# Kernel tuning notes

Hardware: AMD Instinct MI355X
Metric: run time of the kernel (lower is better)

## Reference

```python
import jax, jax.numpy as jnp
import numpy as np

VSN = 1e-12  # VERY_SMALL_NUMBER
B, N, IN_DIM = 48, 512, 400
ENC, HID, OUT, NREL = 256, 128, 128, 53
NUM_PERS, KNN, EPS, SKIP = 4, 10, 0.3, 0.8


def setup_inputs() -> dict:
    key = jax.random.key(0)
    ks = jax.random.split(key, 12)
    context = jax.random.normal(ks[0], (B, N, IN_DIM), dtype=jnp.float32)
    context_lens = jax.random.randint(ks[1], (B,), N // 2, N + 1)
    s1 = jax.random.randint(ks[2], (B,), 0, N - 16)
    e1 = s1 + jax.random.randint(ks[3], (B,), 1, 8)
    s2 = jax.random.randint(ks[4], (B,), 0, N - 16)
    e2 = s2 + jax.random.randint(ks[5], (B,), 1, 8)
    mentions = jnp.stack([s1, e1, s2, e2], axis=-1)  # [B,4]
    sc = lambda d: 1.0 / np.sqrt(d)
    w_enc = jax.random.normal(ks[6], (IN_DIM, ENC), dtype=jnp.float32) * sc(IN_DIM)
    b_enc = jnp.zeros((ENC,), jnp.float32)
    gl_weight = jax.random.normal(ks[7], (NUM_PERS, IN_DIM), dtype=jnp.float32)
    gcn_w1 = jax.random.normal(ks[8], (ENC, HID), dtype=jnp.float32) * sc(ENC)
    gcn_b1 = jnp.zeros((HID,), jnp.float32)
    gcn_w2 = jax.random.normal(ks[9], (HID, OUT), dtype=jnp.float32) * sc(HID)
    gcn_b2 = jnp.zeros((OUT,), jnp.float32)
    lin_w = jax.random.normal(ks[10], (OUT, NREL), dtype=jnp.float32) * sc(OUT)
    lin_b = jnp.zeros((NREL,), jnp.float32)
    return dict(context=context, context_lens=context_lens, mentions=mentions,
                w_enc=w_enc, b_enc=b_enc, gl_weight=gl_weight,
                gcn_w1=gcn_w1, gcn_b1=gcn_b1, gcn_w2=gcn_w2, gcn_b2=gcn_b2,
                lin_w=lin_w, lin_b=lin_b)


def _knn_init_adj(feats, mask):
    # binarized kNN graph on raw features + symmetric normalization
    mask2d = mask[:, :, None] * mask[:, None, :]
    att = jnp.einsum('bnd,bmd->bnm', feats, feats) * mask2d
    _, idx = jax.lax.top_k(att, KNN)                      # [B,N,K]
    adj = jnp.zeros((B, N, N), feats.dtype).at[
        jnp.arange(B)[:, None, None], jnp.arange(N)[None, :, None], idx].set(1.0)
    adj = adj * mask2d
    rowsum = jnp.clip(adj.sum(-1), VSN, None)
    rinv = (rowsum ** -0.5) * mask                        # [B,N]
    return rinv[:, :, None] * adj * rinv[:, None, :]


def _weighted_cosine(feats, gl_weight, mask):
    # multi-perspective weighted cosine similarity, epsilon-sparsified (>=0 adj)
    ctx = feats[None] * gl_weight[:, None, None, :]       # [P,B,N,D]
    ctx = ctx / jnp.clip(jnp.linalg.norm(ctx, axis=-1, keepdims=True), VSN, None)
    att = jnp.einsum('pbnd,pbmd->pbnm', ctx, ctx).mean(0)  # [B,N,N]
    mask2d = mask[:, :, None] * mask[:, None, :]
    att = att * mask2d                                    # markoff_value = 0
    return att * (att > EPS).astype(att.dtype)


def _merge(enc_seq, start, end):
    w_ids = jnp.arange(N)[None, :]                        # [1,N]
    ind = ((w_ids >= start[:, None]) & (w_ids <= end[:, None])).astype(enc_seq.dtype)
    return jnp.einsum('bn,bnd->bd', ind, enc_seq) / ind.sum(-1, keepdims=True)


def reference(context, context_lens, mentions, w_enc, b_enc, gl_weight,
              gcn_w1, gcn_b1, gcn_w2, gcn_b2, lin_w, lin_b):
    mask = (jnp.arange(N)[None, :] < context_lens[:, None]).astype(jnp.float32)
    # init kNN adjacency on detached raw features
    init_adj = _knn_init_adj(jax.lax.stop_gradient(context), mask)
    # context encoder (linear projection stand-in for the LSTM ctx_encoder)
    enc = context @ w_enc + b_enc                          # [B,N,ENC]
    # learned graph: row-normalize then skip-connect with init_adj
    raw_adj = _weighted_cosine(context, gl_weight, mask)
    adj = raw_adj / jnp.clip(raw_adj.sum(-1, keepdims=True), VSN, None)
    adj = SKIP * init_adj + (1.0 - SKIP) * adj
    # 2-hop GCN encoder
    h = jax.nn.relu(jnp.einsum('bnm,bmd->bnd', adj, enc) @ gcn_w1 + gcn_b1)
    node_vec = jnp.einsum('bnm,bmd->bnd', adj, h) @ gcn_w2 + gcn_b2  # [B,N,OUT]
    # graph maxpool over nodes + mention merging (broadcast-mask averaging)
    pooled = node_vec.max(axis=1)                          # [B,OUT]
    arg1 = _merge(node_vec, mentions[:, 0], mentions[:, 1])
    arg2 = _merge(node_vec, mentions[:, 2], mentions[:, 3])
    return (pooled + arg1 + arg2) @ lin_w + lin_b          # [B,NREL]
```

## Files before the change

kernel.cpp:

```cpp
#include <hip/hip_runtime.h>
#include <math.h>

constexpr int cB = 48, cN = 512, cIN = 400;
constexpr int cENC = 256, cHID = 128, cOUT = 128, cNREL = 53;
constexpr int cKNN = 10;
constexpr float cVSN = 1e-12f;
constexpr float cEPS = 0.3f;

constexpr int KP = 416;
constexpr size_t ARRSZ = (size_t)cB * cN * KP;
constexpr int NBN = cB * cN;
constexpr size_t NADJ = (size_t)cB * cN * cN;
constexpr size_t NE1 = (size_t)NBN * 128;

typedef _Float16 f16;
typedef _Float16 f16x8 __attribute__((ext_vector_type(8)));
typedef float f32x4 __attribute__((ext_vector_type(4)));

__device__ inline void gload16(const void* g, void* l) {
    __builtin_amdgcn_global_load_lds(
        (const __attribute__((address_space(1))) unsigned int*)g,
        (__attribute__((address_space(3))) unsigned int*)l, 16, 0, 0);
}

#define MFMA16(a, b, c) __builtin_amdgcn_mfma_f32_16x16x32_f16((a), (b), (c), 0, 0, 0)

__global__ void k_wprep(const float* __restrict__ w_enc, const float* __restrict__ w1,
                        const float* __restrict__ b_enc, const float* __restrict__ w2,
                        f16* __restrict__ wc1H, float* __restrict__ bc1p,
                        f16* __restrict__ w2tH)
{
    int d = blockIdx.x;
    int t = threadIdx.x;
    __shared__ float wred[2][128];
    int o = t & 127, half = t >> 7;
    if (d < cIN) {
        float acc = 0.f;
        const float* we = w_enc + (size_t)d * cENC + half * 128;
        const float* w1p = w1 + (size_t)half * 128 * cHID + o;
        #pragma unroll 8
        for (int e = 0; e < 128; ++e) acc += we[e] * w1p[(size_t)e * cHID];
        wred[half][o] = acc;
        __syncthreads();
        if (half == 0) wc1H[(size_t)o * KP + d] = (f16)(wred[0][o] + wred[1][o]);
    } else if (d < KP) {
        if (t < 128) wc1H[(size_t)o * KP + d] = (f16)0.f;
    } else {
        float acc = 0.f;
        const float* w1p = w1 + (size_t)half * 128 * cHID + o;
        #pragma unroll 8
        for (int e = 0; e < 128; ++e) acc += b_enc[half * 128 + e] * w1p[(size_t)e * cHID];
        wred[half][o] = acc;
        __syncthreads();
        if (half == 0) bc1p[o] = wred[0][o] + wred[1][o];
    }
    if (d < cHID && t < 128) w2tH[(size_t)t * cHID + d] = (f16)w2[(size_t)d * cOUT + t];
}

__global__ __launch_bounds__(256) void k_split(const float* __restrict__ X,
                                               f16* __restrict__ XH, f16* __restrict__ XL)
{
    int t = threadIdx.x;
    int row = blockIdx.x * 4 + (t >> 6);
    int k8 = t & 63;
    if (k8 >= 52) return;
    size_t obase = (size_t)row * KP + k8 * 8;
    if (k8 < 50) {
        const float* x = X + (size_t)row * cIN + k8 * 8;
        float4 xa = *(const float4*)x;
        float4 xb = *(const float4*)(x + 4);
        float xv[8] = {xa.x, xa.y, xa.z, xa.w, xb.x, xb.y, xb.z, xb.w};
        f16x8 vh, vl;
        #pragma unroll
        for (int e = 0; e < 8; ++e) {
            f16 hh = (f16)xv[e];
            vh[e] = hh;
            vl[e] = (f16)(xv[e] - (float)hh);
        }
        *(f16x8*)(XH + obase) = vh;
        *(f16x8*)(XL + obase) = vl;
    } else {
        f16x8 z = (f16x8)(f16)0.f;
        *(f16x8*)(XH + obase) = z;
        *(f16x8*)(XL + obase) = z;
    }
}

__global__ __launch_bounds__(256) void k_norms(const float* __restrict__ X,
                                               const int* __restrict__ lens,
                                               const float* __restrict__ glw,
                                               float* __restrict__ maskA,
                                               float* __restrict__ invnM)
{
    int row = blockIdx.x;
    int t = threadIdx.x;
    int w = t >> 6, lane = t & 63;
    __shared__ float sw[4];
    int b = row >> 9, n = row & (cN - 1);
    float s = 0.f;
    if (lane < 50) {
        int k = lane * 8;
        const float* x = X + (size_t)row * cIN + k;
        const float* g = glw + (size_t)w * cIN + k;
        float4 xa = *(const float4*)x, xb = *(const float4*)(x + 4);
        float4 ga = *(const float4*)g, gb = *(const float4*)(g + 4);
        float xv[8] = {xa.x, xa.y, xa.z, xa.w, xb.x, xb.y, xb.z, xb.w};
        float gv[8] = {ga.x, ga.y, ga.z, ga.w, gb.x, gb.y, gb.z, gb.w};
        #pragma unroll
        for (int e = 0; e < 8; ++e) {
            float tt = xv[e] * gv[e];
            s += tt * tt;
        }
    }
    #pragma unroll
    for (int off = 32; off; off >>= 1) s += __shfl_xor(s, off, 64);
    if (lane == 0) sw[w] = s;
    __syncthreads();
    if (t == 0) {
        float m = (n < lens[b]) ? 1.0f : 0.0f;
        float4 iv;
        iv.x = m / fmaxf(sqrtf(sw[0]), cVSN);
        iv.y = m / fmaxf(sqrtf(sw[1]), cVSN);
        iv.z = m / fmaxf(sqrtf(sw[2]), cVSN);
        iv.w = m / fmaxf(sqrtf(sw[3]), cVSN);
        *(float4*)&invnM[(size_t)row * 4] = iv;
        maskA[row] = m;
    }
}

__global__ __launch_bounds__(256, 3) void k_sim_mfma(
    const f16* __restrict__ XH, const f16* __restrict__ XL,
    const float* __restrict__ glw, const int* __restrict__ lens,
    const float* __restrict__ maskA, const float* __restrict__ invnM,
    float* __restrict__ G0, f16* __restrict__ RAh)
{
    int L = blockIdx.x + (blockIdx.y << 3) + (blockIdx.z << 6);
    int xcd = L & 7, j0 = L >> 3;
    int work = xcd * 384 + j0;
    const int b = work >> 6;
    int rem = work & 63;
    const int n0 = (rem >> 3) * 64, m0 = (rem & 7) * 64;

    const int t = threadIdx.x;
    const int w = t >> 6, lane = t & 63;
    const int wr = w >> 1, wc = w & 1;
    const int lr = lane & 15, lc = lane >> 4;

    const size_t rowBaseB = (size_t)b * cN;
    const int len = lens[b];

    if (n0 >= len || m0 >= len) {
        #pragma unroll
        for (int i = 0; i < 2; ++i)
            #pragma unroll
            for (int jj = 0; jj < 2; ++jj) {
                int m = m0 + wc * 32 + jj * 16 + lr;
                #pragma unroll
                for (int v = 0; v < 4; ++v) {
                    int n = n0 + wr * 32 + i * 16 + lc * 4 + v;
                    size_t rown = rowBaseB + n;
                    __builtin_nontemporal_store(0.f, &G0[rown * cN + m]);
                    RAh[rown * cN + m] = (f16)0.f;
                }
            }
        return;
    }

    __shared__ f16 lds[3][8192];
    __shared__ f16 w2l[4][KP];

    for (int i = t; i < 4 * KP; i += 256) {
        int p = i / KP, d = i - p * KP;
        float g = (d < cIN) ? glw[p * cIN + d] : 0.f;
        w2l[p][d] = (f16)(g * g);
    }

    f32x4 accG[2][2], accP[4][2][2];
    #pragma unroll
    for (int i = 0; i < 2; ++i)
        #pragma unroll
        for (int jj = 0; jj < 2; ++jj) {
            accG[i][jj] = (f32x4)0.f;
            #pragma unroll
            for (int p = 0; p < 4; ++p) accP[p][i][jj] = (f32x4)0.f;
        }

    constexpr int NPAN = KP / 32;

#define SIM_STAGE(buf, pan) do { \
    const int kk0_ = (pan) * 32; \
    _Pragma("unroll") \
    for (int q = 0; q < 4; ++q) { \
        int c_ = w + q * 4;                \
        int tt_ = c_ >> 2, rq_ = c_ & 3; \
        int row_ = rq_ * 16 + (lane >> 2); \
        int kcg_ = (lane & 3) ^ (row_ & 3) ^ ((row_ >> 2) & 3); \
        const f16* arr_ = (tt_ & 1) ? XL : XH; \
        int rb_ = (tt_ < 2) ? n0 : m0; \
        const f16* g_ = arr_ + (rowBaseB + rb_ + row_) * (size_t)KP + kk0_ + kcg_ * 8; \
        gload16(g_, (void*)&lds[buf][tt_ * 2048 + rq_ * 512]); \
    } \
} while (0)

    SIM_STAGE(0, 0);
    SIM_STAGE(1, 1);
    __syncthreads();

    for (int pan = 0; pan < NPAN; ++pan) {
        int cur = pan % 3;
        if (pan + 2 < NPAN) SIM_STAGE((pan + 2) % 3, pan + 2);
        const f16x8* L8 = (const f16x8*)lds[cur];
        const int kk0 = pan * 32;
        f16x8 aH[2], aL[2], bH[2], bL[2], wp[4];
        #pragma unroll
        for (int i = 0; i < 2; ++i) {
            int r = wr * 32 + i * 16 + lr;
            int cell = r * 4 + (lc ^ (r & 3) ^ ((r >> 2) & 3));
            aH[i] = L8[cell];
            aL[i] = L8[256 + cell];
        }
        #pragma unroll
        for (int jj = 0; jj < 2; ++jj) {
            int r = wc * 32 + jj * 16 + lr;
            int cell = r * 4 + (lc ^ (r & 3) ^ ((r >> 2) & 3));
            bH[jj] = L8[512 + cell];
            bL[jj] = L8[768 + cell];
        }
        #pragma unroll
        for (int p = 0; p < 4; ++p) wp[p] = *(const f16x8*)&w2l[p][kk0 + lc * 8];

        __builtin_amdgcn_s_setprio(1);
        #pragma unroll
        for (int i = 0; i < 2; ++i)
            #pragma unroll
            for (int jj = 0; jj < 2; ++jj) {
                accG[i][jj] = MFMA16(aH[i], bH[jj], accG[i][jj]);
                accG[i][jj] = MFMA16(aH[i], bL[jj], accG[i][jj]);
                accG[i][jj] = MFMA16(aL[i], bH[jj], accG[i][jj]);
            }
        #pragma unroll
        for (int p = 0; p < 4; ++p)
            #pragma unroll
            for (int i = 0; i < 2; ++i) {
                f16x8 ap = aH[i] * wp[p];
                #pragma unroll
                for (int jj = 0; jj < 2; ++jj)
                    accP[p][i][jj] = MFMA16(ap, bH[jj], accP[p][i][jj]);
            }
        __builtin_amdgcn_s_setprio(0);

        if (pan < NPAN - 1) {
            if (pan + 2 < NPAN) {
                asm volatile("s_waitcnt vmcnt(4)" ::: "memory");
            } else {
                asm volatile("s_waitcnt vmcnt(0)" ::: "memory");
            }
            asm volatile("s_waitcnt lgkmcnt(0)" ::: "memory");
            __builtin_amdgcn_s_barrier();
        }
    }
#undef SIM_STAGE

    #pragma unroll
    for (int i = 0; i < 2; ++i) {
        #pragma unroll
        for (int jj = 0; jj < 2; ++jj) {
            int m = m0 + wc * 32 + jj * 16 + lr;
            size_t rowm = rowBaseB + m;
            float mskm = maskA[rowm];
            float4 im = *(const float4*)&invnM[rowm * 4];
            #pragma unroll
            for (int v = 0; v < 4; ++v) {
                int n = n0 + wr * 32 + i * 16 + lc * 4 + v;
                size_t rown = rowBaseB + n;
                float4 in_ = *(const float4*)&invnM[rown * 4];
                float g = accG[i][jj][v] * maskA[rown] * mskm;
                float s = 0.25f * (accP[0][i][jj][v] * in_.x * im.x
                                 + accP[1][i][jj][v] * in_.y * im.y
                                 + accP[2][i][jj][v] * in_.z * im.z
                                 + accP[3][i][jj][v] * in_.w * im.w);
                float rv = (s > cEPS) ? s : 0.f;
                __builtin_nontemporal_store(g, &G0[rown * cN + m]);
                RAh[rown * cN + m] = (f16)rv;
            }
        }
    }
}

__global__ void k_topk(const float* __restrict__ G0, const float* __restrict__ mask,
                       const int* __restrict__ lens,
                       int* __restrict__ kidx, float* __restrict__ rinv)
{
    int row = blockIdx.x * 4 + (threadIdx.x >> 6);
    int lane = threadIdx.x & 63;
    int b = row >> 9, n = row & (cN - 1);
    if (n >= lens[b]) {
        if (lane < cKNN) kidx[row * cKNN + lane] = lane;
        if (lane == 0) rinv[row] = 0.f;
        return;
    }
    const float* g = G0 + (long long)row * cN;
    float val[8];
    #pragma unroll
    for (int k = 0; k < 8; ++k)
        val[k] = __builtin_nontemporal_load(&g[lane + 64 * k]);
    float cnt = 0.f;
    long long mbase = (long long)b * cN;
    for (int r = 0; r < cKNN; ++r) {
        float best = val[0];
        #pragma unroll
        for (int k = 1; k < 8; ++k) best = fmaxf(best, val[k]);
        #pragma unroll
        for (int off = 32; off; off >>= 1) best = fmaxf(best, __shfl_xor(best, off, 64));
        int sl = -1;
        #pragma unroll
        for (int k = 7; k >= 0; --k) if (val[k] == best) sl = k;
        unsigned long long holders = __ballot(sl >= 0);
        int src = (int)(__ffsll((long long)holders) - 1);
        int mycol = lane + (sl << 6);
        int col = __shfl(mycol, src, 64);
        if (lane == src) val[sl] = -INFINITY;
        if (lane == 0) {
            kidx[row * cKNN + r] = col;
            cnt += mask[mbase + col];
        }
    }
    if (lane == 0) rinv[row] = rsqrtf(fmaxf(cnt, cVSN));
}

__global__ void k_adj2(const f16* __restrict__ RAh, const float* __restrict__ rinv,
                       const int* __restrict__ kidx, const int* __restrict__ lens,
                       f16* __restrict__ adjH, float* __restrict__ adjrs)
{
    int row = blockIdx.x;
    int t = threadIdx.x;
    int b = row >> 9, n = row & (cN - 1);
    long long base = (long long)row * cN;
    if (n >= lens[b]) {
        *(f16*)&adjH[base + t] = (f16)0.f;
        adjH[base + t + 256] = (f16)0.f;
        if (t == 0) adjrs[row] = 0.f;
        return;
    }
    int w = t >> 6, lane = t & 63;
    __shared__ int sidx[cKNN];
    __shared__ float srv[cKNN];
    __shared__ float red[4];
    long long bbase = (long long)(row & ~(cN - 1));
    if (t < cKNN) {
        int c = kidx[row * cKNN + t];
        sidx[t] = c;
        srv[t] = rinv[bbase + c];
    }
    float ra0 = (float)RAh[base + t];
    float ra1 = (float)RAh[base + t + 256];
    float s = ra0 + ra1;
    #pragma unroll
    for (int off = 32; off; off >>= 1) s += __shfl_xor(s, off, 64);
    if (lane == 0) red[w] = s;
    __syncthreads();
    float rsum = red[0] + red[1] + red[2] + red[3];
    float inv_rs = 1.0f / fmaxf(rsum, cVSN);
    float rn = rinv[row];
    float osum = 0.f;
    #pragma unroll
    for (int mi = 0; mi < 2; ++mi) {
        int m = t + mi * 256;
        float ra = mi ? ra1 : ra0;
        float v = 0.2f * ra * inv_rs;
        #pragma unroll
        for (int k = 0; k < cKNN; ++k)
            if (m == sidx[k]) v += 0.8f * rn * srv[k];
        adjH[base + m] = (f16)v;
        osum += v;
    }
    #pragma unroll
    for (int off = 32; off; off >>= 1) osum += __shfl_xor(osum, off, 64);
    __syncthreads();
    if (lane == 0) red[w] = osum;
    __syncthreads();
    if (t == 0) adjrs[row] = red[0] + red[1] + red[2] + red[3];
}

template<int BIAS, bool RELU, int OMODE, bool ADJA>
__global__ __launch_bounds__(256, 4) void k_gemm1(
    const f16* __restrict__ A, const f16* __restrict__ Bp,
    long long bStrideB, int K, const int* __restrict__ lens,
    const float* __restrict__ biasv, const float* __restrict__ bc1p,
    const float* __restrict__ adjrs, const int* __restrict__ ments,
    f16* __restrict__ CH, float* __restrict__ part)
{
    int L = blockIdx.x + blockIdx.y * gridDim.x;
    int work = (L & 7) * 96 + (L >> 3);
    const int R0 = (work >> 1) * 64;
    const int bn0 = (work & 1) * 64;
    const int bidx = R0 >> 9;
    const int t = threadIdx.x, w = t >> 6, lane = t & 63;
    const int wr = w >> 1, wc = w & 1, lr = lane & 15, lc = lane >> 4;
    __shared__ f16 lds[3][4096];
    __shared__ float sred[2][3][64];
    const f16* Bb = Bp + (size_t)bidx * bStrideB + (size_t)bn0 * K;

    f32x4 acc[2][2];
    #pragma unroll
    for (int i = 0; i < 2; ++i)
        #pragma unroll
        for (int jj = 0; jj < 2; ++jj) acc[i][jj] = (f32x4)0.f;

#define G1_STAGE(buf, p_) do { \
    const int k0_ = (p_) * 32; \
    _Pragma("unroll") \
    for (int q = 0; q < 2; ++q) { \
        int c_ = w + q * 4; \
        int rq_ = c_ & 3; \
        int row_ = rq_ * 16 + (lane >> 2); \
        int kc_ = (lane & 3) ^ (row_ & 3) ^ ((row_ >> 2) & 3); \
        const f16* src_ = (c_ < 4) ? (A + (size_t)(R0 + row_) * K + k0_ + kc_ * 8) \
                                   : (Bb + (size_t)row_ * K + k0_ + kc_ * 8); \
        gload16(src_, (void*)&lds[buf][(c_ >> 2) * 2048 + rq_ * 512]); \
    } \
} while (0)

    int npan = K >> 5;
    bool skipA = false;
    if (ADJA) {
        int lenb = lens[bidx];
        npan = (lenb + 31) >> 5;
        skipA = ((R0 & (cN - 1)) >= lenb);
    }
    if (!skipA) {
        G1_STAGE(0, 0);
        G1_STAGE(1, 1);
        __syncthreads();
        for (int p = 0; p < npan; ++p) {
            int cur = p % 3;
            if (p + 2 < npan) G1_STAGE((p + 2) % 3, p + 2);
            const f16x8* L8 = (const f16x8*)lds[cur];
            f16x8 af[2], bf[2];
            #pragma unroll
            for (int i = 0; i < 2; ++i) {
                int r = wr * 32 + i * 16 + lr;
                int cell = r * 4 + (lc ^ (r & 3) ^ ((r >> 2) & 3));
                af[i] = L8[cell];
            }
            #pragma unroll
            for (int jj = 0; jj < 2; ++jj) {
                int r = wc * 32 + jj * 16 + lr;
                int cell = r * 4 + (lc ^ (r & 3) ^ ((r >> 2) & 3));
                bf[jj] = L8[256 + cell];
            }
            __builtin_amdgcn_s_setprio(1);
            #pragma unroll
            for (int i = 0; i < 2; ++i)
                #pragma unroll
                for (int jj = 0; jj < 2; ++jj)
                    acc[i][jj] = MFMA16(af[i], bf[jj], acc[i][jj]);
            __builtin_amdgcn_s_setprio(0);
            if (p < npan - 1) {
                if (p + 2 < npan) {
                    asm volatile("s_waitcnt vmcnt(2)" ::: "memory");
                } else {
                    asm volatile("s_waitcnt vmcnt(0)" ::: "memory");
                }
                asm volatile("s_waitcnt lgkmcnt(0)" ::: "memory");
                __builtin_amdgcn_s_barrier();
            }
        }
    }
#undef G1_STAGE

    if (OMODE != 2) {
        #pragma unroll
        for (int i = 0; i < 2; ++i)
            #pragma unroll
            for (int jj = 0; jj < 2; ++jj) {
                int col = bn0 + wc * 32 + jj * 16 + lr;
                #pragma unroll
                for (int v = 0; v < 4; ++v) {
                    int r = R0 + wr * 32 + i * 16 + lc * 4 + v;
                    float val = acc[i][jj][v];
                    if (BIAS == 2) val += adjrs[r] * bc1p[col] + biasv[col];
                    if (RELU) val = fmaxf(val, 0.f);
                    size_t addr = (OMODE == 1)
                        ? ((size_t)(r >> 9) * 65536 + (size_t)col * 512 + (r & 511))
                        : ((size_t)r * 128 + col);
                    CH[addr] = (f16)val;
                }
            }
    } else {
        const int b = bidx, rb = (R0 >> 6) & 7, cb = bn0 >> 6;
        int s1 = ments[b * 4 + 0], e1 = ments[b * 4 + 1];
        int s2 = ments[b * 4 + 2], e2 = ments[b * 4 + 3];
        #pragma unroll
        for (int jj = 0; jj < 2; ++jj) {
            int col = bn0 + wc * 32 + jj * 16 + lr;
            float vmax = -INFINITY, v1 = 0.f, v2 = 0.f;
            #pragma unroll
            for (int i = 0; i < 2; ++i)
                #pragma unroll
                for (int v = 0; v < 4; ++v) {
                    int gn = (R0 & 511) + wr * 32 + i * 16 + lc * 4 + v;
                    float val = acc[i][jj][v] + biasv[col];
                    vmax = fmaxf(vmax, val);
                    if (gn >= s1 && gn <= e1) v1 += val;
                    if (gn >= s2 && gn <= e2) v2 += val;
                }
            #pragma unroll
            for (int off = 16; off <= 32; off <<= 1) {
                vmax = fmaxf(vmax, __shfl_xor(vmax, off, 64));
                v1 += __shfl_xor(v1, off, 64);
                v2 += __shfl_xor(v2, off, 64);
            }
            if (lc == 0) {
                int c = wc * 32 + jj * 16 + lr;
                sred[wr][0][c] = vmax;
                sred[wr][1][c] = v1;
                sred[wr][2][c] = v2;
            }
        }
        __syncthreads();
        if (t < 192) {
            int m = t >> 6, c = t & 63;
            float a0 = sred[0][m][c], a1v = sred[1][m][c];
            float comb = (m == 0) ? fmaxf(a0, a1v) : (a0 + a1v);
            part[((((size_t)b * 8 + rb) * 2 + cb) * 3 + m) * 64 + c] = comb;
        }
    }
}

__global__ void k_final2(const float* __restrict__ part, const int* __restrict__ mentions,
                         const float* __restrict__ lw, const float* __restrict__ lb,
                         float* __restrict__ out)
{
    int b = blockIdx.x;
    int t = threadIdx.x;
    __shared__ float vec[128];
    int s1 = mentions[b * 4 + 0], e1 = mentions[b * 4 + 1];
    int s2 = mentions[b * 4 + 2], e2 = mentions[b * 4 + 3];
    int cb = t >> 6, c = t & 63;
    float pm = -INFINITY, s1s = 0.f, s2s = 0.f;
    #pragma unroll
    for (int rb = 0; rb < 8; ++rb) {
        size_t base = ((((size_t)b * 8 + rb) * 2 + cb) * 3) * 64 + c;
        pm = fmaxf(pm, part[base]);
        s1s += part[base + 64];
        s2s += part[base + 128];
    }
    vec[t] = pm + s1s / (float)(e1 - s1 + 1) + s2s / (float)(e2 - s2 + 1);
    __syncthreads();
    if (t < cNREL) {
        float s = lb[t];
        for (int dd = 0; dd < cOUT; ++dd) s += vec[dd] * lw[dd * cNREL + t];
        out[b * cNREL + t] = s;
    }
}

extern "C" void kernel_launch(void* const* d_in, const int* in_sizes, int n_in,
                              void* d_out, int out_size, void* d_ws, size_t ws_size,
                              hipStream_t stream)
{
    const float* context = (const float*)d_in[0];
    const int*   lens    = (const int*)d_in[1];
    const int*   ments   = (const int*)d_in[2];
    const float* w_enc   = (const float*)d_in[3];
    const float* b_enc   = (const float*)d_in[4];
    const float* glw     = (const float*)d_in[5];
    const float* w1      = (const float*)d_in[6];
    const float* b1      = (const float*)d_in[7];
    const float* w2      = (const float*)d_in[8];
    const float* b2      = (const float*)d_in[9];
    const float* lw      = (const float*)d_in[10];
    const float* lb      = (const float*)d_in[11];
    float* out = (float*)d_out;

    f16* XH   = (f16*)d_ws;
    f16* XL   = XH + ARRSZ;
    f16* adjH = XL + ARRSZ;
    f16* E1t  = adjH + NADJ;
    f16* hH   = E1t + NE1;
    f16* H2t  = hH + NE1;
    f16* RAh  = H2t + NE1;
    float* G0 = (float*)(RAh + NADJ);
    float* invnM = G0 + NADJ;
    float* maskA = invnM + 4 * NBN;
    float* rinv  = maskA + NBN;
    float* adjrs = rinv + NBN;
    float* part  = adjrs + NBN;
    float* bc1p  = part + 147456;
    f16* wc1H = (f16*)(bc1p + 128);
    f16* w2tH = wc1H + (size_t)128 * KP;
    int* kidx = (int*)(w2tH + 128 * 128);

    k_wprep<<<KP + 1, 256, 0, stream>>>(w_enc, w1, b_enc, w2, wc1H, bc1p, w2tH);
    k_split<<<NBN / 4, 256, 0, stream>>>(context, XH, XL);
    k_norms<<<NBN, 256, 0, stream>>>(context, lens, glw, maskA, invnM);
    k_sim_mfma<<<dim3(8, 8, cB), 256, 0, stream>>>(XH, XL, glw, lens, maskA, invnM, G0, RAh);
    k_topk<<<NBN / 4, 256, 0, stream>>>(G0, maskA, lens, kidx, rinv);
    k_adj2<<<NBN, 256, 0, stream>>>(RAh, rinv, kidx, lens, adjH, adjrs);

    k_gemm1<0, false, 1, false><<<dim3(NBN / 64, 2), 256, 0, stream>>>(
        XH, wc1H, 0, KP, nullptr, nullptr, nullptr, nullptr, nullptr, E1t, nullptr);
    k_gemm1<2, true, 0, true><<<dim3(NBN / 64, 2), 256, 0, stream>>>(
        adjH, E1t, 65536, cN, lens, b1, bc1p, adjrs, nullptr, hH, nullptr);
    k_gemm1<0, false, 1, false><<<dim3(NBN / 64, 2), 256, 0, stream>>>(
        hH, w2tH, 0, cHID, nullptr, nullptr, nullptr, nullptr, nullptr, H2t, nullptr);
    k_gemm1<0, false, 2, true><<<dim3(NBN / 64, 2), 256, 0, stream>>>(
        adjH, H2t, 65536, cN, lens, b2, nullptr, nullptr, ments, nullptr, part);

    k_final2<<<cB, 128, 0, stream>>>(part, ments, lw, lb, out);
}
```

Measured before the change: 205.3 us.

## Fuse per-tile top-k candidate selection into similarity kernel, drop dense G0 matrix

```diff
diff --git a/kernel.cpp b/kernel.cpp
--- a/kernel.cpp
+++ b/kernel.cpp
@@ -16,6 +16,17 @@
 typedef _Float16 f16;
 typedef _Float16 f16x8 __attribute__((ext_vector_type(8)));
 typedef float f32x4 __attribute__((ext_vector_type(4)));
+
+__device__ inline unsigned long long shfl_xor_u64(unsigned long long v, int off) {
+    int lo = __shfl_xor((int)(unsigned)(v & 0xffffffffull), off, 64);
+    int hi = __shfl_xor((int)(unsigned)(v >> 32), off, 64);
+    return ((unsigned long long)(unsigned)hi << 32) | (unsigned)lo;
+}
+
+__device__ inline unsigned ordf(float v) {
+    unsigned u = __float_as_uint(v);
+    return (u & 0x80000000u) ? ~u : (u | 0x80000000u);
+}
 
 __device__ inline void gload16(const void* g, void* l) {
     __builtin_amdgcn_global_load_lds(
@@ -132,7 +143,7 @@
     const f16* __restrict__ XH, const f16* __restrict__ XL,
     const float* __restrict__ glw, const int* __restrict__ lens,
     const float* __restrict__ maskA, const float* __restrict__ invnM,
-    float* __restrict__ G0, f16* __restrict__ RAh)
+    float2* __restrict__ cand, f16* __restrict__ RAh)
 {
     int L = blockIdx.x + (blockIdx.y << 3) + (blockIdx.z << 6);
     int xcd = L & 7, j0 = L >> 3;
@@ -149,22 +160,7 @@
     const size_t rowBaseB = (size_t)b * cN;
     const int len = lens[b];
 
-    if (n0 >= len || m0 >= len) {
-        #pragma unroll
-        for (int i = 0; i < 2; ++i)
-            #pragma unroll
-            for (int jj = 0; jj < 2; ++jj) {
-                int m = m0 + wc * 32 + jj * 16 + lr;
-                #pragma unroll
-                for (int v = 0; v < 4; ++v) {
-                    int n = n0 + wr * 32 + i * 16 + lc * 4 + v;
-                    size_t rown = rowBaseB + n;
-                    __builtin_nontemporal_store(0.f, &G0[rown * cN + m]);
-                    RAh[rown * cN + m] = (f16)0.f;
-                }
-            }
-        return;
-    }
+    if (n0 >= len || m0 >= len) return;
 
     __shared__ f16 lds[3][8192];
     __shared__ f16 w2l[4][KP];
@@ -261,18 +257,21 @@
     }
 #undef SIM_STAGE
 
+    __syncthreads();
+    float* sG = (float*)lds;
     #pragma unroll
     for (int i = 0; i < 2; ++i) {
         #pragma unroll
         for (int jj = 0; jj < 2; ++jj) {
-            int m = m0 + wc * 32 + jj * 16 + lr;
+            int cl = wc * 32 + jj * 16 + lr;
+            int m = m0 + cl;
             size_t rowm = rowBaseB + m;
             float mskm = maskA[rowm];
             float4 im = *(const float4*)&invnM[rowm * 4];
             #pragma unroll
             for (int v = 0; v < 4; ++v) {
-                int n = n0 + wr * 32 + i * 16 + lc * 4 + v;
-                size_t rown = rowBaseB + n;
+                int rl = wr * 32 + i * 16 + lc * 4 + v;
+                size_t rown = rowBaseB + n0 + rl;
                 float4 in_ = *(const float4*)&invnM[rown * 4];
                 float g = accG[i][jj][v] * maskA[rown] * mskm;
                 float s = 0.25f * (accP[0][i][jj][v] * in_.x * im.x
@@ -280,46 +279,74 @@
                                  + accP[2][i][jj][v] * in_.z * im.z
                                  + accP[3][i][jj][v] * in_.w * im.w);
                 float rv = (s > cEPS) ? s : 0.f;
-                __builtin_nontemporal_store(g, &G0[rown * cN + m]);
+                sG[rl * 66 + cl] = g;
                 RAh[rown * cN + m] = (f16)rv;
             }
         }
     }
-}
-
-__global__ void k_topk(const float* __restrict__ G0, const float* __restrict__ mask,
-                       const int* __restrict__ lens,
-                       int* __restrict__ kidx, float* __restrict__ rinv)
+    __syncthreads();
+
+    int gr = t >> 2, sub = t & 3;
+    size_t crow = (rowBaseB + n0 + gr) * 80 + (size_t)(m0 >> 6) * 10;
+    for (int r = 0; r < cKNN; ++r) {
+        unsigned long long best = 0ull;
+        #pragma unroll
+        for (int c = 0; c < 16; ++c) {
+            int col = sub * 16 + c;
+            float v = sG[gr * 66 + col];
+            unsigned long long kk = ((unsigned long long)ordf(v) << 32) | (unsigned)(63 - col);
+            if (kk > best) best = kk;
+        }
+        unsigned long long o1 = shfl_xor_u64(best, 1);
+        best = (o1 > best) ? o1 : best;
+        unsigned long long o2 = shfl_xor_u64(best, 2);
+        best = (o2 > best) ? o2 : best;
+        int col = 63 - (int)(best & 0xffffffffull);
+        if (sub == 0) {
+            float val = sG[gr * 66 + col];
+            cand[crow + r] = make_float2(val, __int_as_float(m0 + col));
+        }
+        if ((col >> 4) == sub) sG[gr * 66 + col] = -INFINITY;
+    }
+}
+
+__global__ void k_merge(const float2* __restrict__ cand, const float* __restrict__ mask,
+                        const int* __restrict__ lens,
+                        int* __restrict__ kidx, float* __restrict__ rinv)
 {
     int row = blockIdx.x * 4 + (threadIdx.x >> 6);
     int lane = threadIdx.x & 63;
     int b = row >> 9, n = row & (cN - 1);
-    if (n >= lens[b]) {
+    int len = lens[b];
+    if (n >= len) {
         if (lane < cKNN) kidx[row * cKNN + lane] = lane;
         if (lane == 0) rinv[row] = 0.f;
         return;
     }
-    const float* g = G0 + (long long)row * cN;
-    float val[8];
-    #pragma unroll
-    for (int k = 0; k < 8; ++k)
-        val[k] = __builtin_nontemporal_load(&g[lane + 64 * k]);
+    int nval = ((len + 63) >> 6) * 10;
+    unsigned long long key[2];
+    #pragma unroll
+    for (int k = 0; k < 2; ++k) {
+        int e = lane + k * 64;
+        key[k] = 0ull;
+        if (e < nval) {
+            float2 c = cand[(size_t)row * 80 + e];
+            int col = __float_as_int(c.y);
+            key[k] = ((unsigned long long)ordf(c.x) << 32) | (unsigned)(cN - 1 - col);
+        }
+    }
     float cnt = 0.f;
     long long mbase = (long long)b * cN;
     for (int r = 0; r < cKNN; ++r) {
-        float best = val[0];
-        #pragma unroll
-        for (int k = 1; k < 8; ++k) best = fmaxf(best, val[k]);
-        #pragma unroll
-        for (int off = 32; off; off >>= 1) best = fmaxf(best, __shfl_xor(best, off, 64));
-        int sl = -1;
-        #pragma unroll
-        for (int k = 7; k >= 0; --k) if (val[k] == best) sl = k;
-        unsigned long long holders = __ballot(sl >= 0);
-        int src = (int)(__ffsll((long long)holders) - 1);
-        int mycol = lane + (sl << 6);
-        int col = __shfl(mycol, src, 64);
-        if (lane == src) val[sl] = -INFINITY;
+        unsigned long long best = (key[0] > key[1]) ? key[0] : key[1];
+        #pragma unroll
+        for (int off = 32; off; off >>= 1) {
+            unsigned long long o = shfl_xor_u64(best, off);
+            if (o > best) best = o;
+        }
+        int col = (cN - 1) - (int)(best & 0xffffffffull);
+        if (key[0] == best) key[0] = 0ull;
+        if (key[1] == best) key[1] = 0ull;
         if (lane == 0) {
             kidx[row * cKNN + r] = col;
             cnt += mask[mbase + col];
@@ -335,9 +362,10 @@
     int row = blockIdx.x;
     int t = threadIdx.x;
     int b = row >> 9, n = row & (cN - 1);
+    int len = lens[b];
     long long base = (long long)row * cN;
-    if (n >= lens[b]) {
-        *(f16*)&adjH[base + t] = (f16)0.f;
+    if (n >= len) {
+        adjH[base + t] = (f16)0.f;
         adjH[base + t + 256] = (f16)0.f;
         if (t == 0) adjrs[row] = 0.f;
         return;
@@ -352,8 +380,8 @@
         sidx[t] = c;
         srv[t] = rinv[bbase + c];
     }
-    float ra0 = (float)RAh[base + t];
-    float ra1 = (float)RAh[base + t + 256];
+    float ra0 = (t < len) ? (float)RAh[base + t] : 0.f;
+    float ra1 = (t + 256 < len) ? (float)RAh[base + t + 256] : 0.f;
     float s = ra0 + ra1;
     #pragma unroll
     for (int off = 32; off; off >>= 1) s += __shfl_xor(s, off, 64);
@@ -580,8 +608,8 @@
     f16* hH   = E1t + NE1;
     f16* H2t  = hH + NE1;
     f16* RAh  = H2t + NE1;
-    float* G0 = (float*)(RAh + NADJ);
-    float* invnM = G0 + NADJ;
+    float2* cand = (float2*)(RAh + NADJ);
+    float* invnM = (float*)(RAh + NADJ) + NADJ;
     float* maskA = invnM + 4 * NBN;
     float* rinv  = maskA + NBN;
     float* adjrs = rinv + NBN;
@@ -594,8 +622,8 @@
     k_wprep<<<KP + 1, 256, 0, stream>>>(w_enc, w1, b_enc, w2, wc1H, bc1p, w2tH);
     k_split<<<NBN / 4, 256, 0, stream>>>(context, XH, XL);
     k_norms<<<NBN, 256, 0, stream>>>(context, lens, glw, maskA, invnM);
-    k_sim_mfma<<<dim3(8, 8, cB), 256, 0, stream>>>(XH, XL, glw, lens, maskA, invnM, G0, RAh);
-    k_topk<<<NBN / 4, 256, 0, stream>>>(G0, maskA, lens, kidx, rinv);
+    k_sim_mfma<<<dim3(8, 8, cB), 256, 0, stream>>>(XH, XL, glw, lens, maskA, invnM, cand, RAh);
+    k_merge<<<NBN / 4, 256, 0, stream>>>(cand, maskA, lens, kidx, rinv);
     k_adj2<<<NBN, 256, 0, stream>>>(RAh, rinv, kidx, lens, adjH, adjrs);
 
     k_gemm1<0, false, 1, false><<<dim3(NBN / 64, 2), 256, 0, stream>>>(
```

Result: slower. 227.5 us (+10.8%).
